# Performance work log

Hardware: AMD Instinct MI355X
Metric: run time of the kernel (lower is better)

Reference implementation:

```python
import jax, jax.numpy as jnp
import numpy as np

IN_DIM = 128
OUT_DIM = 128
NUM_RELS = 8
N_NODES = 50000
N_EDGES = 500000


def setup_inputs() -> dict:
    key = jax.random.key(0)
    k_x, k_ei_s, k_ei_d, k_et, k_w, k_sw = jax.random.split(key, 6)
    x = jax.random.normal(k_x, (N_NODES, IN_DIM), dtype=jnp.float32)
    src = jax.random.randint(k_ei_s, (N_EDGES,), 0, N_NODES)
    dst = jax.random.randint(k_ei_d, (N_EDGES,), 0, N_NODES)
    edge_index = jnp.stack([src, dst], axis=0).astype(jnp.int64)
    edge_type = jax.random.randint(k_et, (N_EDGES,), 0, NUM_RELS).astype(jnp.int64)
    # xavier_uniform: bound = sqrt(6/(fan_in+fan_out))
    bw = float(np.sqrt(6.0 / (IN_DIM + OUT_DIM)))
    weight = jax.random.uniform(k_w, (NUM_RELS, IN_DIM, OUT_DIM), dtype=jnp.float32, minval=-bw, maxval=bw)
    self_loop_weight = jax.random.uniform(k_sw, (IN_DIM, OUT_DIM), dtype=jnp.float32, minval=-bw, maxval=bw)
    bias = jnp.zeros((OUT_DIM,), dtype=jnp.float32)
    return {
        "x": x,
        "weight": weight,
        "self_loop_weight": self_loop_weight,
        "bias": bias,
        "edge_index": edge_index,
        "edge_type": edge_type,
        "num_entities": N_NODES,
    }


def reference(x, weight, self_loop_weight, bias, edge_index, edge_type, num_entities):
    # Relation-grouped formulation of the per-edge loop:
    # transform every node under every relation once: hr[r, n, o]
    hr = jnp.einsum("nd,rdo->rno", x, weight)
    src, dst = edge_index[0], edge_index[1]
    # per-edge message = x[src] @ weight[edge_type]  == hr[edge_type, src]
    msg = hr[edge_type, src]  # [E, out]
    agg = jax.ops.segment_sum(msg, dst, num_segments=num_entities)  # scatter-add into out[dst]
    out = agg + x @ self_loop_weight + bias
    return jax.nn.relu(out)
```

## Files before the change

### kernel.cpp

```cpp
#include <hip/hip_runtime.h>

#define IN_DIM 128
#define OUT_DIM 128
#define NUM_RELS 8
#define SCAN_ELEMS 2048

typedef unsigned short u16;
typedef u16 u16x8 __attribute__((ext_vector_type(8)));
typedef u16 u16x4 __attribute__((ext_vector_type(4)));
typedef __bf16 bf16x8 __attribute__((ext_vector_type(8)));
typedef float f32x4 __attribute__((ext_vector_type(4)));

__device__ __forceinline__ u16 f2bf(float f) {
    unsigned u = __float_as_uint(f);
    u += 0x7FFF + ((u >> 16) & 1);
    return (u16)(u >> 16);
}
__device__ __forceinline__ float bf2f(u16 h) {
    return __uint_as_float((unsigned)h << 16);
}

__global__ __launch_bounds__(256) void k_prep(
    const float* __restrict__ x, const float* __restrict__ weight,
    const float* __restrict__ slw,
    const int* __restrict__ dst, const int* __restrict__ et,
    u16* __restrict__ xb, u16* __restrict__ WbT, int* __restrict__ cursor,
    int N, int E, int BA, int BB)
{
    const int b = blockIdx.x;
    const int tid = threadIdx.x;
    if (b < BA) {
        long i = ((long)b * 256 + tid) * 4;
        if (i < (long)N * 128) {
            float4 v = *(const float4*)(x + i);
            u16x4 o;
            o[0] = f2bf(v.x); o[1] = f2bf(v.y); o[2] = f2bf(v.z); o[3] = f2bf(v.w);
            *(u16x4*)(xb + i) = o;
        }
    } else if (b < BA + BB) {
        int i = ((b - BA) * 256 + tid) * 4;
        if (i < 128 * 1152) {
            const int col = i / 1152;
            const int kk  = i - col * 1152;
            u16x4 o;
            #pragma unroll
            for (int j = 0; j < 4; ++j) {
                const int kj = kk + j;
                const float f = (kj < 1024)
                    ? weight[((kj >> 7) << 14) + ((kj & 127) << 7) + col]
                    : slw[((kj - 1024) << 7) + col];
                o[j] = f2bf(f);
            }
            *(u16x4*)(WbT + i) = o;
        }
    } else {
        int e = (b - BA - BB) * 256 + tid;
        if (e < E) atomicAdd(&cursor[(dst[e] << 3) + et[e]], 1);
    }
}

__global__ __launch_bounds__(256) void k_scan1(
    const int* __restrict__ deg, int* __restrict__ local,
    int* __restrict__ bsum, int n)
{
    __shared__ int s[256];
    const int t = threadIdx.x;
    const int base = blockIdx.x * SCAN_ELEMS + t * 8;
    int v[8];
    int sum = 0;
    #pragma unroll
    for (int j = 0; j < 8; ++j) {
        int i = base + j;
        v[j] = (i < n) ? deg[i] : 0;
        sum += v[j];
    }
    s[t] = sum;
    __syncthreads();
    #pragma unroll
    for (int off = 1; off < 256; off <<= 1) {
        int y = (t >= off) ? s[t - off] : 0;
        __syncthreads();
        s[t] += y;
        __syncthreads();
    }
    int run = s[t] - sum;
    #pragma unroll
    for (int j = 0; j < 8; ++j) {
        int i = base + j;
        if (i < n) local[i] = run;
        run += v[j];
    }
    if (t == 255) bsum[blockIdx.x] = s[255];
}

__global__ __launch_bounds__(256) void k_scan23(
    int* __restrict__ row_ptr, const int* __restrict__ bsum,
    int* __restrict__ cursor, int B, int n)
{
    __shared__ int s[256];
    const int t = threadIdx.x;
    int v = (t < B) ? bsum[t] : 0;
    s[t] = v;
    __syncthreads();
    #pragma unroll
    for (int off = 1; off < 256; off <<= 1) {
        int y = (t >= off) ? s[t - off] : 0;
        __syncthreads();
        s[t] += y;
        __syncthreads();
    }
    const int myoff = (blockIdx.x == 0) ? 0 : s[blockIdx.x - 1];
    const int total = s[255];
    const int base = blockIdx.x * SCAN_ELEMS + t * 8;
    #pragma unroll
    for (int j = 0; j < 8; ++j) {
        int i = base + j;
        if (i < n) {
            int val = row_ptr[i] + myoff;
            row_ptr[i] = val;
            cursor[i] = val;
        }
    }
    if (blockIdx.x == 0 && t == 0) row_ptr[n] = total;
}

__global__ __launch_bounds__(256) void k_fill(
    const int* __restrict__ src, const int* __restrict__ dst,
    const int* __restrict__ et, int* __restrict__ cursor,
    int* __restrict__ packed, int E)
{
    int e = blockIdx.x * blockDim.x + threadIdx.x;
    if (e >= E) return;
    int pos = atomicAdd(&cursor[(dst[e] << 3) + et[e]], 1);
    packed[pos] = (et[e] << 17) | src[e];
}

#define NPB 64
#define LDK 392

__global__ __launch_bounds__(256, 3) void fused_rgcn(
    const u16* __restrict__ xb,
    const u16* __restrict__ WbT,
    const float* __restrict__ bias,
    const int* __restrict__ row_ptr,
    const int* __restrict__ packed,
    float* __restrict__ out, int N)
{
    __shared__ u16 agg[NPB][LDK];

    const int tid = threadIdx.x;
    const int n0 = blockIdx.x * NPB;
    const int wv = tid >> 6, lane = tid & 63;
    const int q = lane >> 4, l = lane & 15;
    const int cbase = wv << 5;
    const int grp = tid >> 4;
    const int lo  = (tid & 15) * 8;

    f32x4 acc[4][2] = {};

    for (int ck = 0; ck < 3; ++ck) {
        const int r0 = ck * 3;
        const int r1 = (ck == 2) ? 8 : r0 + 3;

        for (int i = 0; i < 4; ++i) {
            const int nl = (grp << 2) + i;
            const int gn = n0 + nl;
            if (gn >= N) break;
            const int beg = row_ptr[(gn << 3) + r0];
            const int end = row_ptr[(gn << 3) + r1];
            u16* arow = &agg[nl][0];
            float a0=0.f,a1=0.f,a2=0.f,a3=0.f,a4=0.f,a5=0.f,a6=0.f,a7=0.f;
            int cur = r0;

#define FLUSH_() { u16x8 o_; \
    o_[0]=f2bf(a0); o_[1]=f2bf(a1); o_[2]=f2bf(a2); o_[3]=f2bf(a3); \
    o_[4]=f2bf(a4); o_[5]=f2bf(a5); o_[6]=f2bf(a6); o_[7]=f2bf(a7); \
    *(u16x8*)(arow + ((cur - r0) << 7) + lo) = o_; \
    a0=0.f;a1=0.f;a2=0.f;a3=0.f;a4=0.f;a5=0.f;a6=0.f;a7=0.f; }

#define PROC_(p_, v_) { const int r_ = (p_) >> 17; \
    while (cur < r_) { FLUSH_(); ++cur; } \
    a0 += bf2f((v_)[0]); a1 += bf2f((v_)[1]); a2 += bf2f((v_)[2]); a3 += bf2f((v_)[3]); \
    a4 += bf2f((v_)[4]); a5 += bf2f((v_)[5]); a6 += bf2f((v_)[6]); a7 += bf2f((v_)[7]); }

            int k = beg;
            for (; k + 8 <= end; k += 8) {
                const int p0 = packed[k],     p1 = packed[k + 1];
                const int p2 = packed[k + 2], p3 = packed[k + 3];
                const int p4 = packed[k + 4], p5 = packed[k + 5];
                const int p6 = packed[k + 6], p7 = packed[k + 7];
                const u16x8 v0 = *(const u16x8*)(xb + (size_t)(p0 & 0x1FFFF) * 128 + lo);
                const u16x8 v1 = *(const u16x8*)(xb + (size_t)(p1 & 0x1FFFF) * 128 + lo);
                const u16x8 v2 = *(const u16x8*)(xb + (size_t)(p2 & 0x1FFFF) * 128 + lo);
                const u16x8 v3 = *(const u16x8*)(xb + (size_t)(p3 & 0x1FFFF) * 128 + lo);
                const u16x8 v4 = *(const u16x8*)(xb + (size_t)(p4 & 0x1FFFF) * 128 + lo);
                const u16x8 v5 = *(const u16x8*)(xb + (size_t)(p5 & 0x1FFFF) * 128 + lo);
                const u16x8 v6 = *(const u16x8*)(xb + (size_t)(p6 & 0x1FFFF) * 128 + lo);
                const u16x8 v7 = *(const u16x8*)(xb + (size_t)(p7 & 0x1FFFF) * 128 + lo);
                PROC_(p0, v0); PROC_(p1, v1); PROC_(p2, v2); PROC_(p3, v3);
                PROC_(p4, v4); PROC_(p5, v5); PROC_(p6, v6); PROC_(p7, v7);
            }
            for (; k + 4 <= end; k += 4) {
                const int p0 = packed[k],     p1 = packed[k + 1];
                const int p2 = packed[k + 2], p3 = packed[k + 3];
                const u16x8 v0 = *(const u16x8*)(xb + (size_t)(p0 & 0x1FFFF) * 128 + lo);
                const u16x8 v1 = *(const u16x8*)(xb + (size_t)(p1 & 0x1FFFF) * 128 + lo);
                const u16x8 v2 = *(const u16x8*)(xb + (size_t)(p2 & 0x1FFFF) * 128 + lo);
                const u16x8 v3 = *(const u16x8*)(xb + (size_t)(p3 & 0x1FFFF) * 128 + lo);
                PROC_(p0, v0); PROC_(p1, v1); PROC_(p2, v2); PROC_(p3, v3);
            }
            for (; k < end; ++k) {
                const int p = packed[k];
                const u16x8 v = *(const u16x8*)(xb + (size_t)(p & 0x1FFFF) * 128 + lo);
                PROC_(p, v);
            }
            while (cur < r1) { FLUSH_(); ++cur; }
            if (ck == 2) {
                const u16x8 sv = *(const u16x8*)(xb + (size_t)gn * 128 + lo);
                *(u16x8*)(arow + 256 + lo) = sv;
            }
#undef PROC_
#undef FLUSH_
        }
        __syncthreads();

        const u16* B0p = WbT + (size_t)(cbase + l) * 1152 + ck * 384 + (q << 3);
        const u16* B1p = B0p + (size_t)16 * 1152;

        #pragma unroll
        for (int kk = 0; kk < 12; ++kk) {
            const int k0 = (kk << 5) + (q << 3);
            const bf16x8 b0 = __builtin_bit_cast(bf16x8, *(const u16x8*)(B0p + (kk << 5)));
            const bf16x8 b1 = __builtin_bit_cast(bf16x8, *(const u16x8*)(B1p + (kk << 5)));
            const bf16x8 a0 = __builtin_bit_cast(bf16x8, *(const u16x8*)(&agg[l][k0]));
            const bf16x8 a1 = __builtin_bit_cast(bf16x8, *(const u16x8*)(&agg[16 + l][k0]));
            const bf16x8 a2 = __builtin_bit_cast(bf16x8, *(const u16x8*)(&agg[32 + l][k0]));
            const bf16x8 a3 = __builtin_bit_cast(bf16x8, *(const u16x8*)(&agg[48 + l][k0]));
            acc[0][0] = __builtin_amdgcn_mfma_f32_16x16x32_bf16(a0, b0, acc[0][0], 0, 0, 0);
            acc[0][1] = __builtin_amdgcn_mfma_f32_16x16x32_bf16(a0, b1, acc[0][1], 0, 0, 0);
            acc[1][0] = __builtin_amdgcn_mfma_f32_16x16x32_bf16(a1, b0, acc[1][0], 0, 0, 0);
            acc[1][1] = __builtin_amdgcn_mfma_f32_16x16x32_bf16(a1, b1, acc[1][1], 0, 0, 0);
            acc[2][0] = __builtin_amdgcn_mfma_f32_16x16x32_bf16(a2, b0, acc[2][0], 0, 0, 0);
            acc[2][1] = __builtin_amdgcn_mfma_f32_16x16x32_bf16(a2, b1, acc[2][1], 0, 0, 0);
            acc[3][0] = __builtin_amdgcn_mfma_f32_16x16x32_bf16(a3, b0, acc[3][0], 0, 0, 0);
            acc[3][1] = __builtin_amdgcn_mfma_f32_16x16x32_bf16(a3, b1, acc[3][1], 0, 0, 0);
        }
        if (ck < 2) __syncthreads();
    }

    const float bv0 = bias[cbase + l];
    const float bv1 = bias[cbase + 16 + l];
    const int rbase = n0 + (q << 2);
    #pragma unroll
    for (int mt = 0; mt < 4; ++mt) {
        const int row = rbase + (mt << 4);
        #pragma unroll
        for (int j = 0; j < 4; ++j) {
            if (row + j < N) {
                float* op = out + (size_t)(row + j) * 128 + cbase + l;
                op[0]  = fmaxf(acc[mt][0][j] + bv0, 0.f);
                op[16] = fmaxf(acc[mt][1][j] + bv1, 0.f);
            }
        }
    }
}

__global__ __launch_bounds__(256) void gemm128(
    const float* __restrict__ x, const float* __restrict__ W,
    const float* __restrict__ bias, float* __restrict__ out, int N)
{
    __shared__ float Ws[IN_DIM * OUT_DIM];
    __shared__ float xs[16][IN_DIM];

    const float* Wz = W + (size_t)blockIdx.z * IN_DIM * OUT_DIM;
    float* outz = out + (size_t)blockIdx.z * (size_t)N * OUT_DIM;

    {
        const float4* s4 = (const float4*)Wz;
        float4* d4 = (float4*)Ws;
        for (int i = threadIdx.x; i < IN_DIM * OUT_DIM / 4; i += 256)
            d4[i] = s4[i];
    }

    const int tid = threadIdx.x;
    const int nl = (tid >> 5) * 2;
    const int og = (tid & 31) * 4;

    float4 b4 = make_float4(0.f, 0.f, 0.f, 0.f);
    if (bias) b4 = *(const float4*)&bias[og];

    const int nchunks = (N + 15) / 16;
    for (int chunk = blockIdx.x; chunk < nchunks; chunk += gridDim.x) {
        const int n0 = chunk * 16;
        const int rows = min(16, N - n0);
        __syncthreads();
        {
            const float4* xsrc = (const float4*)(x + (size_t)n0 * IN_DIM);
            float4* xdst = (float4*)&xs[0][0];
            const int n4 = rows * (IN_DIM / 4);
            for (int i = tid; i < n4; i += 256) xdst[i] = xsrc[i];
        }
        __syncthreads();

        if (nl < rows) {
            float a00 = 0.f, a01 = 0.f, a02 = 0.f, a03 = 0.f;
            float a10 = 0.f, a11 = 0.f, a12 = 0.f, a13 = 0.f;
            #pragma unroll 8
            for (int d = 0; d < IN_DIM; ++d) {
                const float4 w4 = *(const float4*)&Ws[d * OUT_DIM + og];
                const float xa = xs[nl][d];
                const float xb = xs[nl + 1][d];
                a00 += xa * w4.x; a01 += xa * w4.y; a02 += xa * w4.z; a03 += xa * w4.w;
                a10 += xb * w4.x; a11 += xb * w4.y; a12 += xb * w4.z; a13 += xb * w4.w;
            }
            float4 r0 = make_float4(a00 + b4.x, a01 + b4.y, a02 + b4.z, a03 + b4.w);
            *(float4*)&outz[(size_t)(n0 + nl) * OUT_DIM + og] = r0;
            if (nl + 1 < rows) {
                float4 r1 = make_float4(a10 + b4.x, a11 + b4.y, a12 + b4.z, a13 + b4.w);
                *(float4*)&outz[(size_t)(n0 + nl + 1) * OUT_DIM + og] = r1;
            }
        }
    }
}

__global__ __launch_bounds__(256) void edge_direct(
    const float* __restrict__ x, const float* __restrict__ W,
    const int* __restrict__ src, const int* __restrict__ dst,
    const int* __restrict__ et, float* __restrict__ out, int E)
{
    long t = (long)blockIdx.x * blockDim.x + threadIdx.x;
    long e = t >> 6;
    int lane = (int)(t & 63);
    if (e >= E) return;
    int s = src[e], d = dst[e], r = et[e];
    const float* xr = x + (long)s * IN_DIM;
    float2 xv = *(const float2*)(xr + lane * 2);
    const float* Wr = W + (long)r * IN_DIM * OUT_DIM;
    const int o0 = lane * 2;
    float a0 = 0.f, a1 = 0.f;
    #pragma unroll 8
    for (int dd = 0; dd < 64; ++dd) {
        float xa = __shfl(xv.x, dd);
        float xb = __shfl(xv.y, dd);
        a0 += xa * Wr[(2 * dd) * OUT_DIM + o0]     + xb * Wr[(2 * dd + 1) * OUT_DIM + o0];
        a1 += xa * Wr[(2 * dd) * OUT_DIM + o0 + 1] + xb * Wr[(2 * dd + 1) * OUT_DIM + o0 + 1];
    }
    atomicAdd(out + (long)d * OUT_DIM + o0, a0);
    atomicAdd(out + (long)d * OUT_DIM + o0 + 1, a1);
}

__global__ __launch_bounds__(256) void relu_k(float* __restrict__ out, long n4)
{
    long i = (long)blockIdx.x * blockDim.x + threadIdx.x;
    if (i >= n4) return;
    float4 v = ((float4*)out)[i];
    v.x = fmaxf(v.x, 0.f); v.y = fmaxf(v.y, 0.f);
    v.z = fmaxf(v.z, 0.f); v.w = fmaxf(v.w, 0.f);
    ((float4*)out)[i] = v;
}

static inline size_t align256(size_t x) { return (x + 255) & ~(size_t)255; }

extern "C" void kernel_launch(void* const* d_in, const int* in_sizes, int n_in,
                              void* d_out, int out_size, void* d_ws, size_t ws_size,
                              hipStream_t stream)
{
    const float* x      = (const float*)d_in[0];
    const float* weight = (const float*)d_in[1];
    const float* slw    = (const float*)d_in[2];
    const float* bias   = (const float*)d_in[3];
    const int*   ei     = (const int*)d_in[4];
    const int*   et     = (const int*)d_in[5];

    const int N = in_sizes[0] / IN_DIM;
    const int E = in_sizes[5];
    const int* src  = ei;
    const int* dstp = ei + E;

    float* out = (float*)d_out;

    const int n8 = N * 8;

    size_t off = 0;
    const size_t xb_off   = off; off += align256((size_t)N * 128 * 2);
    const size_t wb_off   = off; off += align256((size_t)128 * 1152 * 2);
    const size_t rp_off   = off; off += align256((size_t)(n8 + 1) * 4);
    const size_t cur_off  = off; off += align256((size_t)n8 * 4);
    const size_t pk_off   = off; off += align256((size_t)E * 4);
    const size_t bs_off   = off; off += align256(256 * 4);
    const size_t need_bf16 = off;

    const int scanB = (n8 + SCAN_ELEMS - 1) / SCAN_ELEMS;

    if (ws_size >= need_bf16 && N <= (1 << 17) && scanB <= 256) {
        char* base   = (char*)d_ws;
        u16* xb      = (u16*)(base + xb_off);
        u16* WbT     = (u16*)(base + wb_off);
        int* row_ptr = (int*)(base + rp_off);
        int* cursor  = (int*)(base + cur_off);
        int* packed  = (int*)(base + pk_off);
        int* bsum    = (int*)(base + bs_off);

        hipMemsetAsync(cursor, 0, (size_t)n8 * sizeof(int), stream);
        const int BA = (int)(((long)N * 128 / 4 + 255) / 256);
        const int BB = (128 * 1152 / 4 + 255) / 256;
        const int BD = (E + 255) / 256;
        k_prep<<<dim3(BA + BB + BD), 256, 0, stream>>>(
            x, weight, slw, dstp, et, xb, WbT, cursor, N, E, BA, BB);

        k_scan1<<<dim3(scanB), 256, 0, stream>>>(cursor, row_ptr, bsum, n8);
        k_scan23<<<dim3(scanB), 256, 0, stream>>>(row_ptr, bsum, cursor, scanB, n8);
        k_fill<<<dim3((E + 255) / 256), 256, 0, stream>>>(src, dstp, et, cursor, packed, E);

        fused_rgcn<<<dim3((N + NPB - 1) / NPB), 256, 0, stream>>>(
            xb, WbT, bias, row_ptr, packed, out, N);
    } else if (ws_size >= (size_t)NUM_RELS * N * 128 * 4) {
        gemm128<<<dim3(512, 1, 1), 256, 0, stream>>>(x, slw, bias, out, N);
        long nt = (long)E * 64;
        edge_direct<<<dim3((nt + 255) / 256), 256, 0, stream>>>(x, weight, src, dstp, et, out, E);
        long n4 = (long)N * OUT_DIM / 4;
        relu_k<<<dim3((n4 + 255) / 256), 256, 0, stream>>>(out, n4);
    } else {
        gemm128<<<dim3(512, 1, 1), 256, 0, stream>>>(x, slw, bias, out, N);
        long nt = (long)E * 64;
        edge_direct<<<dim3((nt + 255) / 256), 256, 0, stream>>>(x, weight, src, dstp, et, out, E);
        long n4 = (long)N * OUT_DIM / 4;
        relu_k<<<dim3((n4 + 255) / 256), 256, 0, stream>>>(out, n4);
    }
}
```

Baseline: 251.9 us.

## Use one node per 16-thread group with 512-thread blocks of 32 nodes

The fused aggregation+GEMM kernel now processes 32 nodes per block with 512 threads. Each 16-lane group gathers one node's edges instead of four, and each wave computes a 16-column slice instead of 32 in the MFMA stage. This raises gather parallelism and occupancy to hide the latency of irregular neighbor loads. It also drops the 8-wide unrolled edge loop. The cost is that each block loads a larger share of the weight matrix per node and the MFMA work per wave is smaller.

New measurement: 225.2 us. -10.6%, faster.

```diff
diff --git a/kernel.cpp b/kernel.cpp
--- a/kernel.cpp
+++ b/kernel.cpp
@@ -135,10 +135,10 @@
     packed[pos] = (et[e] << 17) | src[e];
 }
 
-#define NPB 64
+#define NPB 32
 #define LDK 392
 
-__global__ __launch_bounds__(256, 3) void fused_rgcn(
+__global__ __launch_bounds__(512, 8) void fused_rgcn(
     const u16* __restrict__ xb,
     const u16* __restrict__ WbT,
     const float* __restrict__ bias,
@@ -150,25 +150,25 @@
 
     const int tid = threadIdx.x;
     const int n0 = blockIdx.x * NPB;
-    const int wv = tid >> 6, lane = tid & 63;
+    const int lane = tid & 63;
+    const int wv = tid >> 6;
     const int q = lane >> 4, l = lane & 15;
-    const int cbase = wv << 5;
+    const int cbase = wv << 4;
     const int grp = tid >> 4;
     const int lo  = (tid & 15) * 8;
 
-    f32x4 acc[4][2] = {};
+    const int gn = n0 + grp;
+    u16* arow = &agg[grp][0];
+
+    f32x4 acc[2] = {};
 
     for (int ck = 0; ck < 3; ++ck) {
         const int r0 = ck * 3;
         const int r1 = (ck == 2) ? 8 : r0 + 3;
 
-        for (int i = 0; i < 4; ++i) {
-            const int nl = (grp << 2) + i;
-            const int gn = n0 + nl;
-            if (gn >= N) break;
+        if (gn < N) {
             const int beg = row_ptr[(gn << 3) + r0];
             const int end = row_ptr[(gn << 3) + r1];
-            u16* arow = &agg[nl][0];
             float a0=0.f,a1=0.f,a2=0.f,a3=0.f,a4=0.f,a5=0.f,a6=0.f,a7=0.f;
             int cur = r0;
 
@@ -184,39 +184,23 @@
     a4 += bf2f((v_)[4]); a5 += bf2f((v_)[5]); a6 += bf2f((v_)[6]); a7 += bf2f((v_)[7]); }
 
             int k = beg;
-            for (; k + 8 <= end; k += 8) {
-                const int p0 = packed[k],     p1 = packed[k + 1];
-                const int p2 = packed[k + 2], p3 = packed[k + 3];
-                const int p4 = packed[k + 4], p5 = packed[k + 5];
-                const int p6 = packed[k + 6], p7 = packed[k + 7];
-                const u16x8 v0 = *(const u16x8*)(xb + (size_t)(p0 & 0x1FFFF) * 128 + lo);
-                const u16x8 v1 = *(const u16x8*)(xb + (size_t)(p1 & 0x1FFFF) * 128 + lo);
-                const u16x8 v2 = *(const u16x8*)(xb + (size_t)(p2 & 0x1FFFF) * 128 + lo);
-                const u16x8 v3 = *(const u16x8*)(xb + (size_t)(p3 & 0x1FFFF) * 128 + lo);
-                const u16x8 v4 = *(const u16x8*)(xb + (size_t)(p4 & 0x1FFFF) * 128 + lo);
-                const u16x8 v5 = *(const u16x8*)(xb + (size_t)(p5 & 0x1FFFF) * 128 + lo);
-                const u16x8 v6 = *(const u16x8*)(xb + (size_t)(p6 & 0x1FFFF) * 128 + lo);
-                const u16x8 v7 = *(const u16x8*)(xb + (size_t)(p7 & 0x1FFFF) * 128 + lo);
-                PROC_(p0, v0); PROC_(p1, v1); PROC_(p2, v2); PROC_(p3, v3);
-                PROC_(p4, v4); PROC_(p5, v5); PROC_(p6, v6); PROC_(p7, v7);
-            }
             for (; k + 4 <= end; k += 4) {
                 const int p0 = packed[k],     p1 = packed[k + 1];
                 const int p2 = packed[k + 2], p3 = packed[k + 3];
-                const u16x8 v0 = *(const u16x8*)(xb + (size_t)(p0 & 0x1FFFF) * 128 + lo);
-                const u16x8 v1 = *(const u16x8*)(xb + (size_t)(p1 & 0x1FFFF) * 128 + lo);
-                const u16x8 v2 = *(const u16x8*)(xb + (size_t)(p2 & 0x1FFFF) * 128 + lo);
-                const u16x8 v3 = *(const u16x8*)(xb + (size_t)(p3 & 0x1FFFF) * 128 + lo);
+                const u16x8 v0 = *(const u16x8*)(xb + ((size_t)(p0 & 0x1FFFF) << 7) + lo);
+                const u16x8 v1 = *(const u16x8*)(xb + ((size_t)(p1 & 0x1FFFF) << 7) + lo);
+                const u16x8 v2 = *(const u16x8*)(xb + ((size_t)(p2 & 0x1FFFF) << 7) + lo);
+                const u16x8 v3 = *(const u16x8*)(xb + ((size_t)(p3 & 0x1FFFF) << 7) + lo);
                 PROC_(p0, v0); PROC_(p1, v1); PROC_(p2, v2); PROC_(p3, v3);
             }
             for (; k < end; ++k) {
                 const int p = packed[k];
-                const u16x8 v = *(const u16x8*)(xb + (size_t)(p & 0x1FFFF) * 128 + lo);
+                const u16x8 v = *(const u16x8*)(xb + ((size_t)(p & 0x1FFFF) << 7) + lo);
                 PROC_(p, v);
             }
             while (cur < r1) { FLUSH_(); ++cur; }
             if (ck == 2) {
-                const u16x8 sv = *(const u16x8*)(xb + (size_t)gn * 128 + lo);
+                const u16x8 sv = *(const u16x8*)(xb + ((size_t)gn << 7) + lo);
                 *(u16x8*)(arow + 256 + lo) = sv;
             }
 #undef PROC_
@@ -224,43 +208,28 @@
         }
         __syncthreads();
 
-        const u16* B0p = WbT + (size_t)(cbase + l) * 1152 + ck * 384 + (q << 3);
-        const u16* B1p = B0p + (size_t)16 * 1152;
-
+        const u16* Bp = WbT + (size_t)(cbase + l) * 1152 + ck * 384 + (q << 3);
         #pragma unroll
         for (int kk = 0; kk < 12; ++kk) {
             const int k0 = (kk << 5) + (q << 3);
-            const bf16x8 b0 = __builtin_bit_cast(bf16x8, *(const u16x8*)(B0p + (kk << 5)));
-            const bf16x8 b1 = __builtin_bit_cast(bf16x8, *(const u16x8*)(B1p + (kk << 5)));
+            const bf16x8 b  = __builtin_bit_cast(bf16x8, *(const u16x8*)(Bp + (kk << 5)));
             const bf16x8 a0 = __builtin_bit_cast(bf16x8, *(const u16x8*)(&agg[l][k0]));
             const bf16x8 a1 = __builtin_bit_cast(bf16x8, *(const u16x8*)(&agg[16 + l][k0]));
-            const bf16x8 a2 = __builtin_bit_cast(bf16x8, *(const u16x8*)(&agg[32 + l][k0]));
-            const bf16x8 a3 = __builtin_bit_cast(bf16x8, *(const u16x8*)(&agg[48 + l][k0]));
-            acc[0][0] = __builtin_amdgcn_mfma_f32_16x16x32_bf16(a0, b0, acc[0][0], 0, 0, 0);
-            acc[0][1] = __builtin_amdgcn_mfma_f32_16x16x32_bf16(a0, b1, acc[0][1], 0, 0, 0);
-            acc[1][0] = __builtin_amdgcn_mfma_f32_16x16x32_bf16(a1, b0, acc[1][0], 0, 0, 0);
-            acc[1][1] = __builtin_amdgcn_mfma_f32_16x16x32_bf16(a1, b1, acc[1][1], 0, 0, 0);
-            acc[2][0] = __builtin_amdgcn_mfma_f32_16x16x32_bf16(a2, b0, acc[2][0], 0, 0, 0);
-            acc[2][1] = __builtin_amdgcn_mfma_f32_16x16x32_bf16(a2, b1, acc[2][1], 0, 0, 0);
-            acc[3][0] = __builtin_amdgcn_mfma_f32_16x16x32_bf16(a3, b0, acc[3][0], 0, 0, 0);
-            acc[3][1] = __builtin_amdgcn_mfma_f32_16x16x32_bf16(a3, b1, acc[3][1], 0, 0, 0);
+            acc[0] = __builtin_amdgcn_mfma_f32_16x16x32_bf16(a0, b, acc[0], 0, 0, 0);
+            acc[1] = __builtin_amdgcn_mfma_f32_16x16x32_bf16(a1, b, acc[1], 0, 0, 0);
         }
         if (ck < 2) __syncthreads();
     }
 
-    const float bv0 = bias[cbase + l];
-    const float bv1 = bias[cbase + 16 + l];
-    const int rbase = n0 + (q << 2);
-    #pragma unroll
-    for (int mt = 0; mt < 4; ++mt) {
-        const int row = rbase + (mt << 4);
+    const float bv = bias[cbase + l];
+    #pragma unroll
+    for (int m = 0; m < 2; ++m) {
+        const int rbase = n0 + (m << 4) + (q << 2);
         #pragma unroll
         for (int j = 0; j < 4; ++j) {
-            if (row + j < N) {
-                float* op = out + (size_t)(row + j) * 128 + cbase + l;
-                op[0]  = fmaxf(acc[mt][0][j] + bv0, 0.f);
-                op[16] = fmaxf(acc[mt][1][j] + bv1, 0.f);
-            }
+            const int row = rbase + j;
+            if (row < N)
+                out[(size_t)row * 128 + cbase + l] = fmaxf(acc[m][j] + bv, 0.f);
         }
     }
 }
@@ -412,7 +381,7 @@
         k_scan23<<<dim3(scanB), 256, 0, stream>>>(row_ptr, bsum, cursor, scanB, n8);
         k_fill<<<dim3((E + 255) / 256), 256, 0, stream>>>(src, dstp, et, cursor, packed, E);
 
-        fused_rgcn<<<dim3((N + NPB - 1) / NPB), 256, 0, stream>>>(
+        fused_rgcn<<<dim3((N + NPB - 1) / NPB), 512, 0, stream>>>(
             xb, WbT, bias, row_ptr, packed, out, N);
     } else if (ws_size >= (size_t)NUM_RELS * N * 128 * 4) {
         gemm128<<<dim3(512, 1, 1), 256, 0, stream>>>(x, slw, bias, out, N);
```
